# Optimization experiments

Measured on AMD Instinct MI355X. Metric: run time of the kernel, lower is better.

The kernel has to match this reference:

```python
import jax, jax.numpy as jnp
import numpy as np

VOCAB = 10000
EMBED = 300
BATCH = 262144
X_MAX = 100.0
ALPHA = 0.75


def setup_inputs() -> dict:
    key = jax.random.key(0)
    k1, k2, k3, k4, k5, k6, k7 = jax.random.split(key, 7)
    # embeddings / biases initialized uniform(-0.5, 0.5) like the torch module
    V = jax.random.uniform(k1, (VOCAB, EMBED), jnp.float32, -0.5, 0.5)
    U = jax.random.uniform(k2, (VOCAB, EMBED), jnp.float32, -0.5, 0.5)
    v_bias = jax.random.uniform(k3, (VOCAB,), jnp.float32, -0.5, 0.5)
    u_bias = jax.random.uniform(k4, (VOCAB,), jnp.float32, -0.5, 0.5)
    # dense co-occurrence matrix; strictly positive, spans the x < x_max branch
    comat = jax.random.uniform(k5, (VOCAB, VOCAB), jnp.float32) * 150.0 + 1e-3
    center_word_lookup = jax.random.randint(k6, (BATCH,), 0, VOCAB, jnp.int32)
    context_word_lookup = jax.random.randint(k7, (BATCH,), 0, VOCAB, jnp.int32)
    return {
        "center_word_lookup": center_word_lookup,
        "context_word_lookup": context_word_lookup,
        "V": V,
        "U": U,
        "v_bias": v_bias,
        "u_bias": u_bias,
        "comat": comat,
    }


def reference(center_word_lookup, context_word_lookup, V, U, v_bias, u_bias, comat):
    # embedding gathers: [B, E] and [B]
    center_embed = V[center_word_lookup]
    target_embed = U[context_word_lookup]
    center_bias = v_bias[center_word_lookup]
    target_bias = u_bias[context_word_lookup]
    # co-occurrence counts for each (i, j) pair: [B]
    x = comat[center_word_lookup, context_word_lookup]
    # GloVe weighting f(x) = (x / x_max)^alpha if x < x_max else 1
    weights = jnp.where(x < X_MAX, (x / X_MAX) ** ALPHA, 1.0)
    # dot(v_i, u_j) + b_i + b_j - log(X_ij)
    dots = jnp.einsum("be,be->b", center_embed, target_embed)
    residual = dots + center_bias + target_bias - jnp.log(x)
    return jnp.sum(weights * residual * residual)
```

## Files before the change

kernel.cpp:

```cpp
#include <hip/hip_runtime.h>

#define VOCAB 10000
#define EMBED 300

__global__ __launch_bounds__(256) void glove_kernel(
    const int* __restrict__ center, const int* __restrict__ context,
    const float* __restrict__ V, const float* __restrict__ U,
    const float* __restrict__ vb, const float* __restrict__ ub,
    const float* __restrict__ comat, float* __restrict__ out, int batch)
{
    const int lane16 = threadIdx.x & 15;
    const int group  = threadIdx.x >> 4;
    const int gpb    = blockDim.x >> 4;
    const int gid    = blockIdx.x * gpb + group;
    const int ngroups = gridDim.x * gpb;

    float total = 0.f;
    for (int b = gid; b < batch; b += ngroups) {
        const int i = center[b];
        const int j = context[b];
        const float4* __restrict__ Vrow = (const float4*)(V + (size_t)i * EMBED);
        const float4* __restrict__ Urow = (const float4*)(U + (size_t)j * EMBED);
        float dot = 0.f;
#pragma unroll
        for (int k = 0; k < 5; ++k) {
            const int idx = lane16 + 16 * k;
            if (idx < 75) {
                float4 a = Vrow[idx];
                float4 c = Urow[idx];
                dot = fmaf(a.x, c.x, dot);
                dot = fmaf(a.y, c.y, dot);
                dot = fmaf(a.z, c.z, dot);
                dot = fmaf(a.w, c.w, dot);
            }
        }
#pragma unroll
        for (int off = 8; off > 0; off >>= 1)
            dot += __shfl_down(dot, off, 16);
        if (lane16 == 0) {
            const float x = comat[(size_t)i * VOCAB + j];
            const float w = (x < 100.0f) ? __powf(x * 0.01f, 0.75f) : 1.0f;
            const float r = dot + vb[i] + ub[j] - __logf(x);
            total = fmaf(w * r, r, total);
        }
    }

#pragma unroll
    for (int off = 32; off > 0; off >>= 1)
        total += __shfl_down(total, off, 64);

    __shared__ float smem[4];
    const int wave = threadIdx.x >> 6;
    const int lane = threadIdx.x & 63;
    if (lane == 0) smem[wave] = total;
    __syncthreads();
    if (threadIdx.x == 0) {
        float s = smem[0] + smem[1] + smem[2] + smem[3];
        atomicAdd(out, s);
    }
}

extern "C" void kernel_launch(void* const* d_in, const int* in_sizes, int n_in,
                              void* d_out, int out_size, void* d_ws, size_t ws_size,
                              hipStream_t stream) {
    const int*   center  = (const int*)d_in[0];
    const int*   context = (const int*)d_in[1];
    const float* V       = (const float*)d_in[2];
    const float* U       = (const float*)d_in[3];
    const float* vb      = (const float*)d_in[4];
    const float* ub      = (const float*)d_in[5];
    const float* comat   = (const float*)d_in[6];
    float* out = (float*)d_out;

    const int batch = in_sizes[0];

    hipMemsetAsync(out, 0, sizeof(float), stream);

    dim3 grid(1024), block(256);
    glove_kernel<<<grid, block, 0, stream>>>(center, context, V, U, vb, ub,
                                             comat, out, batch);
}
```

Before: 534.6 us.

## Hoist comat load before dot product, raise grid size, use two-pass reduction

The comat gather now issues at the start of each iteration, in every lane, so its latency overlaps the V/U row loads instead of waiting until after the shuffle reduction. The grid grows from 1024 to 4096 blocks to put more memory requests in flight. The atomicAdd and memset are replaced by per-block partials in the workspace plus a single-block reduce kernel. In exchange, every lane now loads comat redundantly (same address, so the loads coalesce), and there is an extra kernel launch.

```diff
diff --git a/kernel.cpp b/kernel.cpp
--- a/kernel.cpp
+++ b/kernel.cpp
@@ -2,12 +2,13 @@
 
 #define VOCAB 10000
 #define EMBED 300
+#define NBLOCKS 4096
 
 __global__ __launch_bounds__(256) void glove_kernel(
     const int* __restrict__ center, const int* __restrict__ context,
     const float* __restrict__ V, const float* __restrict__ U,
     const float* __restrict__ vb, const float* __restrict__ ub,
-    const float* __restrict__ comat, float* __restrict__ out, int batch)
+    const float* __restrict__ comat, float* __restrict__ partials, int batch)
 {
     const int lane16 = threadIdx.x & 15;
     const int group  = threadIdx.x >> 4;
@@ -19,6 +20,7 @@
     for (int b = gid; b < batch; b += ngroups) {
         const int i = center[b];
         const int j = context[b];
+        const float x = comat[(size_t)i * VOCAB + j];
         const float4* __restrict__ Vrow = (const float4*)(V + (size_t)i * EMBED);
         const float4* __restrict__ Urow = (const float4*)(U + (size_t)j * EMBED);
         float dot = 0.f;
@@ -38,7 +40,6 @@
         for (int off = 8; off > 0; off >>= 1)
             dot += __shfl_down(dot, off, 16);
         if (lane16 == 0) {
-            const float x = comat[(size_t)i * VOCAB + j];
             const float w = (x < 100.0f) ? __powf(x * 0.01f, 0.75f) : 1.0f;
             const float r = dot + vb[i] + ub[j] - __logf(x);
             total = fmaf(w * r, r, total);
@@ -54,10 +55,27 @@
     const int lane = threadIdx.x & 63;
     if (lane == 0) smem[wave] = total;
     __syncthreads();
-    if (threadIdx.x == 0) {
-        float s = smem[0] + smem[1] + smem[2] + smem[3];
-        atomicAdd(out, s);
-    }
+    if (threadIdx.x == 0)
+        partials[blockIdx.x] = smem[0] + smem[1] + smem[2] + smem[3];
+}
+
+__global__ __launch_bounds__(256) void reduce_kernel(
+    const float* __restrict__ partials, float* __restrict__ out, int n)
+{
+    float s = 0.f;
+    for (int k = threadIdx.x; k < n; k += 256)
+        s += partials[k];
+#pragma unroll
+    for (int off = 32; off > 0; off >>= 1)
+        s += __shfl_down(s, off, 64);
+
+    __shared__ float smem[4];
+    const int wave = threadIdx.x >> 6;
+    const int lane = threadIdx.x & 63;
+    if (lane == 0) smem[wave] = s;
+    __syncthreads();
+    if (threadIdx.x == 0)
+        out[0] = smem[0] + smem[1] + smem[2] + smem[3];
 }
 
 extern "C" void kernel_launch(void* const* d_in, const int* in_sizes, int n_in,
@@ -70,13 +88,12 @@
     const float* vb      = (const float*)d_in[4];
     const float* ub      = (const float*)d_in[5];
     const float* comat   = (const float*)d_in[6];
-    float* out = (float*)d_out;
+    float* out      = (float*)d_out;
+    float* partials = (float*)d_ws;
 
     const int batch = in_sizes[0];
 
-    hipMemsetAsync(out, 0, sizeof(float), stream);
-
-    dim3 grid(1024), block(256);
-    glove_kernel<<<grid, block, 0, stream>>>(center, context, V, U, vb, ub,
-                                             comat, out, batch);
+    glove_kernel<<<dim3(NBLOCKS), dim3(256), 0, stream>>>(
+        center, context, V, U, vb, ub, comat, partials, batch);
+    reduce_kernel<<<dim3(1), dim3(256), 0, stream>>>(partials, out, NBLOCKS);
 }
```

New measurement: 529.6 us. No clear change (-0.9%).
